# Kernel optimization log

Measured on AMD Instinct MI355X. Metric: run time of the kernel, lower is better.

The kernel has to match this reference:

```python
import jax, jax.numpy as jnp
import numpy as np

N_USERS = 100000
N_ITEMS = 50000
N_NODES = N_USERS + N_ITEMS
D = 32
N_EDGES = 8000000
N_LAYERS = 3
B = 65536


def setup_inputs() -> dict:
    key = jax.random.key(0)
    ks = jax.random.split(key, 9)
    users = jax.random.randint(ks[0], (B,), 0, N_USERS)
    items = jax.random.randint(ks[1], (B,), 0, N_ITEMS)
    # COO sparse normalized adjacency (symmetric bipartite graph in LightGCN)
    rows = jax.random.randint(ks[2], (N_EDGES,), 0, N_NODES)
    cols = jax.random.randint(ks[3], (N_EDGES,), 0, N_NODES)
    # normalized values ~ 1/sqrt(deg_i*deg_j); keep small so propagation is stable
    vals = jax.random.uniform(ks[4], (N_EDGES,), dtype=jnp.float32) * 0.01
    # embedding tables, init std=0.1 per nn.init.normal_(std=0.1)
    user_emb = jax.random.normal(ks[5], (N_USERS, D), dtype=jnp.float32) * 0.1
    item_emb = jax.random.normal(ks[6], (N_ITEMS, D), dtype=jnp.float32) * 0.1
    # per-user denormalization stats (norm_mode='users')
    norm_means = jax.random.normal(ks[7], (N_USERS,), dtype=jnp.float32)
    norm_stds = jax.random.uniform(ks[8], (N_USERS,), dtype=jnp.float32) + 0.5
    return {
        "users": users, "items": items,
        "rows": rows, "cols": cols, "vals": vals,
        "user_emb": user_emb, "item_emb": item_emb,
        "norm_means": norm_means, "norm_stds": norm_stds,
    }


def _spmm(rows, cols, vals, x):
    # sparse COO matmul: out[i] = sum_{e: rows[e]==i} vals[e] * x[cols[e]]
    return jax.ops.segment_sum(vals[:, None] * x[cols], rows, num_segments=N_NODES)


def reference(users, items, rows, cols, vals, user_emb, item_emb, norm_means, norm_stds):
    all_emb = jnp.concatenate([user_emb, item_emb], axis=0)  # [N, D]
    acc = all_emb
    emb_sum = all_emb
    for _ in range(N_LAYERS):
        acc = _spmm(rows, cols, vals, acc)
        emb_sum = emb_sum + acc
    light_out = emb_sum / jnp.asarray(N_LAYERS + 1, dtype=all_emb.dtype)
    all_users = light_out[:N_USERS]
    all_items = light_out[N_USERS:]
    gamma = jnp.sum(all_users[users] * all_items[items], axis=1)  # [B]
    # norm_mode == 'users' -> index stats by users
    return gamma * norm_stds[users] + norm_means[users]
```

## Files before the change

### kernel.cpp

```cpp
#include <hip/hip_runtime.h>
#include <hip/hip_fp16.h>

#define N_USERS 100000
#define N_ITEMS 50000
#define N_NODES 150000
#define DIM 32
#define N_EDGES 8000000
#define B_OUT 65536

#define NB 1024
#define RPB 147
#define CH 8192
#define N_PBLK ((N_EDGES + CH - 1) / CH)
#define PART_T 1024
#define EPT (CH / PART_T)
#define MS_T 1024
#define T 256
#define NRED 8
#define NPANEL 3
#define NBIN (RPB * NPANEL)
#define BUFE 8448
#define VQ_SCALE 1638400.0f
#define VQ_INV   6.103515625e-7f
#define WSCALE1 (VQ_INV * 8.0f)
#define WSCALE2 (VQ_INV * 32.0f)
#define WSCALE3 (VQ_INV * 32.0f)
#define INV1 (1.0f / 64.0f)
#define INV2 (1.0f / 2048.0f)
#define INV3 (1.0f / 65536.0f)

__device__ __forceinline__ unsigned enc_h(unsigned u16) {
    return (u16 + 0x7Fu + ((u16 >> 8) & 1u)) >> 8;
}
__device__ __forceinline__ unsigned enc_f(float x) {
    return enc_h((unsigned)__half_as_ushort(__float2half(x)));
}
__device__ __forceinline__ float dec_b(unsigned b) {
    return __half2float(__ushort_as_half((unsigned short)(b << 8)));
}
__device__ __forceinline__ int panel_of(int col) {
    return (col >= 100000) ? 2 : ((col >= 50000) ? 1 : 0);
}
__device__ __forceinline__ int chend(int c) {
    int e = (c + 1) * CH;
    return (e > N_EDGES) ? N_EDGES : e;
}

__global__ void init_kernel(const float* __restrict__ user_emb,
                            const float* __restrict__ item_emb,
                            unsigned char* __restrict__ x_a) {
    int i = blockIdx.x * blockDim.x + threadIdx.x;
    const int total = N_NODES * DIM / 8;
    if (i >= total) return;
    const int user8 = N_USERS * DIM / 8;
    const float4* src = (i < user8) ? ((const float4*)user_emb + (size_t)i * 2)
                                    : ((const float4*)item_emb + (size_t)(i - user8) * 2);
    float4 a = src[0], b = src[1];
    unsigned w0 = enc_f(a.x * 8.f) | (enc_f(a.y * 8.f) << 8)
                | (enc_f(a.z * 8.f) << 16) | (enc_f(a.w * 8.f) << 24);
    unsigned w1 = enc_f(b.x * 8.f) | (enc_f(b.y * 8.f) << 8)
                | (enc_f(b.z * 8.f) << 16) | (enc_f(b.w * 8.f) << 24);
    uint2 o; o.x = w0; o.y = w1;
    ((uint2*)x_a)[i] = o;
}

__global__ void __launch_bounds__(PART_T)
part_kernel(const int* __restrict__ rows,
            const int* __restrict__ cols,
            const float* __restrict__ vals,
            int* __restrict__ rsA,
            int2* __restrict__ bucket_ev) {
    __shared__ int2 buf[CH];
    __shared__ int hist[NB];
    __shared__ int wsum[16];
    const int tid   = threadIdx.x;
    const int chunk = blockIdx.x;
    const int e0    = chunk * CH;
    const int ecnt  = (N_EDGES - e0 < CH) ? (N_EDGES - e0) : CH;
    const int lane  = tid & 63, wid = tid >> 6;

    hist[tid] = 0;
    __syncthreads();

    int myrow[EPT];
    #pragma unroll
    for (int j = 0; j < EPT; ++j) {
        int idx = j * PART_T + tid;
        int r = (idx < ecnt) ? rows[e0 + idx] : -1;
        myrow[j] = r;
        if (r >= 0) atomicAdd(&hist[(unsigned)r / RPB], 1);
    }
    __syncthreads();

    int v = hist[tid];
    int inc = v;
    #pragma unroll
    for (int off = 1; off < 64; off <<= 1) {
        int t = __shfl_up(inc, off, 64);
        if (lane >= off) inc += t;
    }
    if (lane == 63) wsum[wid] = inc;
    __syncthreads();
    if (wid == 0) {
        int s = (lane < 16) ? wsum[lane] : 0;
        #pragma unroll
        for (int off = 1; off < 16; off <<= 1) {
            int t = __shfl_up(s, off, 64);
            if (lane >= off) s += t;
        }
        if (lane < 16) wsum[lane] = s;
    }
    __syncthreads();
    int base = (wid > 0) ? wsum[wid - 1] : 0;
    int excl = base + inc - v;
    rsA[(size_t)chunk * NB + tid] = e0 + excl;
    hist[tid] = excl;
    __syncthreads();

    #pragma unroll
    for (int j = 0; j < EPT; ++j) {
        int r = myrow[j];
        if (r < 0) continue;
        int idx = j * PART_T + tid;
        unsigned b = (unsigned)r / RPB;
        int k = atomicAdd(&hist[b], 1);
        int2 ev;
        ev.x = (int)(((unsigned)(r - (int)b * RPB) << 18) | (unsigned)cols[e0 + idx]);
        ev.y = __float_as_int(vals[e0 + idx]);
        buf[k] = ev;
    }
    __syncthreads();

    const int n4 = ecnt >> 1;
    const int4* b4 = (const int4*)buf;
    int4* g4 = (int4*)(bucket_ev + e0);
    for (int i = tid; i < n4; i += PART_T) g4[i] = b4[i];
}

__global__ void transpose_kernel(const int* __restrict__ in, int* __restrict__ out) {
    __shared__ int t[32][33];
    const int c0 = blockIdx.x * 32, b0 = blockIdx.y * 32;
    for (int dy = threadIdx.y; dy < 32; dy += 8) {
        int c = c0 + dy, b = b0 + threadIdx.x;
        t[dy][threadIdx.x] = (c < N_PBLK) ? in[(size_t)c * NB + b] : 0;
    }
    __syncthreads();
    for (int dy = threadIdx.y; dy < 32; dy += 8) {
        int b = b0 + dy, c = c0 + threadIdx.x;
        if (c < N_PBLK) out[(size_t)b * N_PBLK + c] = t[threadIdx.x][dy];
    }
}

__global__ void btot_kernel(const int* __restrict__ rsA, int* __restrict__ partial) {
    const int b = threadIdx.x;
    const int g = blockIdx.x;
    int c = 0;
    for (int ch = g; ch < N_PBLK; ch += NRED) {
        int s0 = rsA[(size_t)ch * NB + b];
        int s1 = (b < NB - 1) ? rsA[(size_t)ch * NB + b + 1] : chend(ch);
        c += s1 - s0;
    }
    partial[g * NB + b] = c;
}

__global__ void bscan_kernel(const int* __restrict__ partial,
                             int* __restrict__ bcsr,
                             int* __restrict__ row_ptr) {
    __shared__ int wsum[16];
    const int tid = threadIdx.x;
    const int lane = tid & 63, wid = tid >> 6;
    int v = 0;
    #pragma unroll
    for (int g = 0; g < NRED; ++g) v += partial[g * NB + tid];
    int inc = v;
    #pragma unroll
    for (int off = 1; off < 64; off <<= 1) {
        int t = __shfl_up(inc, off, 64);
        if (lane >= off) inc += t;
    }
    if (lane == 63) wsum[wid] = inc;
    __syncthreads();
    if (wid == 0) {
        int s = (lane < 16) ? wsum[lane] : 0;
        #pragma unroll
        for (int off = 1; off < 16; off <<= 1) {
            int t = __shfl_up(s, off, 64);
            if (lane >= off) s += t;
        }
        if (lane < 16) wsum[lane] = s;
    }
    __syncthreads();
    int base = (wid > 0) ? wsum[wid - 1] : 0;
    bcsr[tid] = base + inc - v;
    if (tid == 0) row_ptr[N_NODES] = N_EDGES;
}

__global__ void __launch_bounds__(MS_T)
mini_scatter_kernel(const int* __restrict__ rsT,
                    const int2* __restrict__ bucket_ev,
                    const int* __restrict__ bcsr,
                    int* __restrict__ row_ptr,
                    unsigned* __restrict__ csr_w) {
    __shared__ int2 ibuf[BUFE];
    __shared__ unsigned sbuf[BUFE];
    __shared__ int rs0[N_PBLK];
    __shared__ int ofs[N_PBLK];
    __shared__ int rlen[N_PBLK];
    __shared__ int cnt2[NBIN];
    __shared__ int cur2[NBIN];
    __shared__ int wsum[MS_T / 64];
    const int b   = blockIdx.x;
    const int tid = threadIdx.x;
    const int lane = tid & 63, wid = tid >> 6;

    for (int i = tid; i < N_PBLK; i += MS_T) {
        int a = rsT[(size_t)b * N_PBLK + i];
        int e = (b < NB - 1) ? rsT[(size_t)(b + 1) * N_PBLK + i]
                             : chend(i);
        rs0[i]  = a;
        rlen[i] = e - a;
    }
    if (tid < NBIN) cnt2[tid] = 0;
    __syncthreads();

    int lv = (tid < N_PBLK) ? rlen[tid] : 0;
    int linc = lv;
    #pragma unroll
    for (int off = 1; off < 64; off <<= 1) {
        int t = __shfl_up(linc, off, 64);
        if (lane >= off) linc += t;
    }
    if (lane == 63) wsum[wid] = linc;
    __syncthreads();
    if (wid == 0) {
        int s = (lane < MS_T / 64) ? wsum[lane] : 0;
        #pragma unroll
        for (int off = 1; off < MS_T / 64; off <<= 1) {
            int t = __shfl_up(s, off, 64);
            if (lane >= off) s += t;
        }
        if (lane < MS_T / 64) wsum[lane] = s;
    }
    __syncthreads();
    int lbase = (wid > 0) ? wsum[wid - 1] : 0;
    if (tid < N_PBLK) ofs[tid] = lbase + linc - lv;
    __syncthreads();
    const int cnt = ofs[N_PBLK - 1] + rlen[N_PBLK - 1];
    __syncthreads();

    const int grp8 = tid >> 3, ln8 = tid & 7;
    const int cb = bcsr[b];

    if (cnt <= BUFE) {
        for (int c = grp8; c < N_PBLK; c += (MS_T / 8)) {
            int s0 = rs0[c], o0 = ofs[c], L = rlen[c];
            for (int i = ln8; i < L; i += 8) ibuf[o0 + i] = bucket_ev[s0 + i];
        }
        __syncthreads();
        for (int i = tid; i < cnt; i += MS_T) {
            unsigned key = (unsigned)ibuf[i].x;
            atomicAdd(&cnt2[((int)(key >> 18)) * NPANEL + panel_of((int)(key & 0x3FFFFu))], 1);
        }
    } else {
        for (int c = grp8; c < N_PBLK; c += (MS_T / 8)) {
            int s0 = rs0[c], L = rlen[c];
            for (int i = ln8; i < L; i += 8) {
                unsigned key = (unsigned)bucket_ev[s0 + i].x;
                atomicAdd(&cnt2[((int)(key >> 18)) * NPANEL + panel_of((int)(key & 0x3FFFFu))], 1);
            }
        }
    }
    __syncthreads();

    int v = (tid < NBIN) ? cnt2[tid] : 0;
    int inc = v;
    #pragma unroll
    for (int off = 1; off < 64; off <<= 1) {
        int t = __shfl_up(inc, off, 64);
        if (lane >= off) inc += t;
    }
    if (lane == 63) wsum[wid] = inc;
    __syncthreads();
    if (wid == 0) {
        int s = (lane < MS_T / 64) ? wsum[lane] : 0;
        #pragma unroll
        for (int off = 1; off < MS_T / 64; off <<= 1) {
            int t = __shfl_up(s, off, 64);
            if (lane >= off) s += t;
        }
        if (lane < MS_T / 64) wsum[lane] = s;
    }
    __syncthreads();
    int base = (wid > 0) ? wsum[wid - 1] : 0;
    if (tid < NBIN) {
        int excl = base + inc - v;
        cur2[tid] = excl;
        if (tid % NPANEL == 0) {
            int r = b * RPB + tid / NPANEL;
            if (r < N_NODES) row_ptr[r] = cb + excl;
        }
    }
    __syncthreads();

    if (cnt <= BUFE) {
        for (int i = tid; i < cnt; i += MS_T) {
            int2 ev = ibuf[i];
            unsigned key = (unsigned)ev.x;
            int rl  = (int)(key >> 18);
            int col = (int)(key & 0x3FFFFu);
            float vv = __int_as_float(ev.y);
            int q = (int)(vv * VQ_SCALE + 0.5f);
            if (q > 16383) q = 16383;
            int pos = atomicAdd(&cur2[rl * NPANEL + panel_of(col)], 1);
            sbuf[pos] = ((unsigned)col << 14) | (unsigned)q;
        }
        __syncthreads();
        unsigned* g = csr_w + cb;
        for (int i = tid; i < cnt; i += MS_T) g[i] = sbuf[i];
    } else {
        for (int c = grp8; c < N_PBLK; c += (MS_T / 8)) {
            int s0 = rs0[c], L = rlen[c];
            for (int i = ln8; i < L; i += 8) {
                int2 ev = bucket_ev[s0 + i];
                unsigned key = (unsigned)ev.x;
                int rl  = (int)(key >> 18);
                int col = (int)(key & 0x3FFFFu);
                float vv = __int_as_float(ev.y);
                int q = (int)(vv * VQ_SCALE + 0.5f);
                if (q > 16383) q = 16383;
                int pos = atomicAdd(&cur2[rl * NPANEL + panel_of(col)], 1);
                csr_w[cb + pos] = ((unsigned)col << 14) | (unsigned)q;
            }
        }
    }
}

__global__ void spmm_kernel(const int* __restrict__ row_ptr,
                            const unsigned* __restrict__ csr,
                            const unsigned char* __restrict__ xin,
                            unsigned char* __restrict__ xout,
                            float wscale) {
    int tid = blockIdx.x * blockDim.x + threadIdx.x;
    int row = tid >> 5;
    if (row >= N_NODES) return;
    const int ll  = tid & 31;
    const int j   = ll >> 2;
    const int seg = ll & 3;
    const int s = row_ptr[row];
    const int e = row_ptr[row + 1];
    const unsigned char* xseg = xin + seg * 8;

    __half2 acc0 = __float2half2_rn(0.f);
    __half2 acc1 = acc0, acc2 = acc0, acc3 = acc0;

    for (int i = s; i < e; i += 32) {
        int e0 = i + j, e1 = i + 8 + j, e2 = i + 16 + j, e3 = i + 24 + j;
        unsigned p0 = (e0 < e) ? csr[e0] : 0u;
        unsigned p1 = (e1 < e) ? csr[e1] : 0u;
        unsigned p2 = (e2 < e) ? csr[e2] : 0u;
        unsigned p3 = (e3 < e) ? csr[e3] : 0u;
        uint2 v0 = *(const uint2*)(xseg + ((size_t)((p0 >> 9) & ~31u)));
        uint2 v1 = *(const uint2*)(xseg + ((size_t)((p1 >> 9) & ~31u)));
        uint2 v2 = *(const uint2*)(xseg + ((size_t)((p2 >> 9) & ~31u)));
        uint2 v3 = *(const uint2*)(xseg + ((size_t)((p3 >> 9) & ~31u)));
        __half2 w0 = __float2half2_rn((float)(p0 & 0x3FFFu) * wscale);
        __half2 w1 = __float2half2_rn((float)(p1 & 0x3FFFu) * wscale);
        __half2 w2 = __float2half2_rn((float)(p2 & 0x3FFFu) * wscale);
        __half2 w3 = __float2half2_rn((float)(p3 & 0x3FFFu) * wscale);
        unsigned h;
        h = __builtin_amdgcn_perm(v0.x, v0.x, 0x010C000Cu);
        acc0 = __hfma2(w0, *(__half2*)&h, acc0);
        h = __builtin_amdgcn_perm(v0.x, v0.x, 0x030C020Cu);
        acc1 = __hfma2(w0, *(__half2*)&h, acc1);
        h = __builtin_amdgcn_perm(v0.y, v0.y, 0x010C000Cu);
        acc2 = __hfma2(w0, *(__half2*)&h, acc2);
        h = __builtin_amdgcn_perm(v0.y, v0.y, 0x030C020Cu);
        acc3 = __hfma2(w0, *(__half2*)&h, acc3);
        h = __builtin_amdgcn_perm(v1.x, v1.x, 0x010C000Cu);
        acc0 = __hfma2(w1, *(__half2*)&h, acc0);
        h = __builtin_amdgcn_perm(v1.x, v1.x, 0x030C020Cu);
        acc1 = __hfma2(w1, *(__half2*)&h, acc1);
        h = __builtin_amdgcn_perm(v1.y, v1.y, 0x010C000Cu);
        acc2 = __hfma2(w1, *(__half2*)&h, acc2);
        h = __builtin_amdgcn_perm(v1.y, v1.y, 0x030C020Cu);
        acc3 = __hfma2(w1, *(__half2*)&h, acc3);
        h = __builtin_amdgcn_perm(v2.x, v2.x, 0x010C000Cu);
        acc0 = __hfma2(w2, *(__half2*)&h, acc0);
        h = __builtin_amdgcn_perm(v2.x, v2.x, 0x030C020Cu);
        acc1 = __hfma2(w2, *(__half2*)&h, acc1);
        h = __builtin_amdgcn_perm(v2.y, v2.y, 0x010C000Cu);
        acc2 = __hfma2(w2, *(__half2*)&h, acc2);
        h = __builtin_amdgcn_perm(v2.y, v2.y, 0x030C020Cu);
        acc3 = __hfma2(w2, *(__half2*)&h, acc3);
        h = __builtin_amdgcn_perm(v3.x, v3.x, 0x010C000Cu);
        acc0 = __hfma2(w3, *(__half2*)&h, acc0);
        h = __builtin_amdgcn_perm(v3.x, v3.x, 0x030C020Cu);
        acc1 = __hfma2(w3, *(__half2*)&h, acc1);
        h = __builtin_amdgcn_perm(v3.y, v3.y, 0x010C000Cu);
        acc2 = __hfma2(w3, *(__half2*)&h, acc2);
        h = __builtin_amdgcn_perm(v3.y, v3.y, 0x030C020Cu);
        acc3 = __hfma2(w3, *(__half2*)&h, acc3);
    }

    #pragma unroll
    for (int m = 4; m <= 16; m <<= 1) {
        unsigned t;
        t = (unsigned)__shfl_xor(*(int*)&acc0, m, 64); acc0 = __hadd2(acc0, *(__half2*)&t);
        t = (unsigned)__shfl_xor(*(int*)&acc1, m, 64); acc1 = __hadd2(acc1, *(__half2*)&t);
        t = (unsigned)__shfl_xor(*(int*)&acc2, m, 64); acc2 = __hadd2(acc2, *(__half2*)&t);
        t = (unsigned)__shfl_xor(*(int*)&acc3, m, 64); acc3 = __hadd2(acc3, *(__half2*)&t);
    }

    if (j == 0) {
        unsigned a0 = *(unsigned*)&acc0, a1 = *(unsigned*)&acc1;
        unsigned a2 = *(unsigned*)&acc2, a3 = *(unsigned*)&acc3;
        unsigned w0 = enc_h(a0 & 0xFFFFu) | (enc_h(a0 >> 16) << 8)
                    | (enc_h(a1 & 0xFFFFu) << 16) | (enc_h(a1 >> 16) << 24);
        unsigned w1 = enc_h(a2 & 0xFFFFu) | (enc_h(a2 >> 16) << 8)
                    | (enc_h(a3 & 0xFFFFu) << 16) | (enc_h(a3 >> 16) << 24);
        uint2 o; o.x = w0; o.y = w1;
        *(uint2*)(xout + (size_t)row * 32 + seg * 8) = o;
    }
}

__device__ __forceinline__ void add_row8(float* s, const unsigned char* x,
                                         size_t node, float inv) {
    const uint4* p = (const uint4*)(x + node * 32);
    uint4 t0 = p[0], t1 = p[1];
    unsigned w[8] = {t0.x, t0.y, t0.z, t0.w, t1.x, t1.y, t1.z, t1.w};
    #pragma unroll
    for (int k = 0; k < 8; ++k) {
        unsigned ww = w[k];
        s[k * 4 + 0] += dec_b(ww & 0xFFu) * inv;
        s[k * 4 + 1] += dec_b((ww >> 8) & 0xFFu) * inv;
        s[k * 4 + 2] += dec_b((ww >> 16) & 0xFFu) * inv;
        s[k * 4 + 3] += dec_b(ww >> 24) * inv;
    }
}

__global__ void final_kernel(const int* __restrict__ users,
                             const int* __restrict__ items,
                             const float* __restrict__ user_emb,
                             const float* __restrict__ item_emb,
                             const unsigned char* __restrict__ x1,
                             const unsigned char* __restrict__ x2,
                             const unsigned char* __restrict__ x3,
                             const float* __restrict__ means,
                             const float* __restrict__ stds,
                             float* __restrict__ out) {
    int b = blockIdx.x * blockDim.x + threadIdx.x;
    if (b >= B_OUT) return;
    int u  = users[b];
    int itm = items[b];
    size_t un = (size_t)u;
    size_t in = (size_t)(N_USERS + itm);

    float su[DIM], si[DIM];
    const float4* eu = (const float4*)(user_emb + un * DIM);
    const float4* ei = (const float4*)(item_emb + (size_t)itm * DIM);
    #pragma unroll
    for (int k = 0; k < 8; ++k) {
        float4 a = eu[k];
        su[k * 4 + 0] = a.x; su[k * 4 + 1] = a.y; su[k * 4 + 2] = a.z; su[k * 4 + 3] = a.w;
        float4 c = ei[k];
        si[k * 4 + 0] = c.x; si[k * 4 + 1] = c.y; si[k * 4 + 2] = c.z; si[k * 4 + 3] = c.w;
    }
    add_row8(su, x1, un, INV1); add_row8(su, x2, un, INV2); add_row8(su, x3, un, INV3);
    add_row8(si, x1, in, INV1); add_row8(si, x2, in, INV2); add_row8(si, x3, in, INV3);

    float gamma = 0.f;
    #pragma unroll
    for (int d = 0; d < DIM; ++d) gamma += su[d] * si[d];
    gamma *= 0.0625f;
    out[b] = gamma * stds[u] + means[u];
}

extern "C" void kernel_launch(void* const* d_in, const int* in_sizes, int n_in,
                              void* d_out, int out_size, void* d_ws, size_t ws_size,
                              hipStream_t stream) {
    const int*   users    = (const int*)d_in[0];
    const int*   items    = (const int*)d_in[1];
    const int*   rows     = (const int*)d_in[2];
    const int*   cols     = (const int*)d_in[3];
    const float* vals     = (const float*)d_in[4];
    const float* user_emb = (const float*)d_in[5];
    const float* item_emb = (const float*)d_in[6];
    const float* means    = (const float*)d_in[7];
    const float* stds     = (const float*)d_in[8];
    float* out = (float*)d_out;

    char* w = (char*)d_ws;
    size_t off = 0;
    auto alloc = [&](size_t bytes) -> void* {
        void* p = w + off;
        off = (off + bytes + 255) & ~(size_t)255;
        return p;
    };
    size_t regionA = ((size_t)N_PBLK * CH * sizeof(int2) + 255) & ~(size_t)255;
    char* a0 = (char*)alloc(regionA);
    int2* bucket_ev = (int2*)a0;
    size_t aoff = 0;
    auto allocA = [&](size_t bytes) -> void* {
        void* p = a0 + aoff;
        aoff = (aoff + bytes + 255) & ~(size_t)255;
        return p;
    };
    unsigned char* x_a = (unsigned char*)allocA((size_t)N_NODES * DIM);
    unsigned char* x_b = (unsigned char*)allocA((size_t)N_NODES * DIM);
    unsigned char* x_c = (unsigned char*)allocA((size_t)N_NODES * DIM);
    unsigned char* x_d = (unsigned char*)allocA((size_t)N_NODES * DIM);

    int*      rsA     = (int*)     alloc((size_t)N_PBLK * NB * sizeof(int));
    int*      rsT     = (int*)     alloc((size_t)NB * N_PBLK * sizeof(int));
    int*      partial = (int*)     alloc((size_t)NRED * NB * sizeof(int));
    int*      row_ptr = (int*)     alloc((size_t)(N_NODES + 1) * sizeof(int));
    int*      bcsr    = (int*)     alloc((size_t)NB * sizeof(int));
    unsigned* csr_w   = (unsigned*)alloc((size_t)N_EDGES * sizeof(unsigned));
    (void)ws_size;

    const int g_init  = (N_NODES * DIM / 8 + T - 1) / T;
    const int g_spmm  = (N_NODES * DIM + T - 1) / T;
    const int g_final = (B_OUT + T - 1) / T;

    part_kernel<<<N_PBLK, PART_T, 0, stream>>>(rows, cols, vals, rsA, bucket_ev);
    dim3 tgrid((N_PBLK + 31) / 32, NB / 32);
    transpose_kernel<<<tgrid, dim3(32, 8), 0, stream>>>(rsA, rsT);
    btot_kernel<<<NRED, NB, 0, stream>>>(rsA, partial);
    bscan_kernel<<<1, NB, 0, stream>>>(partial, bcsr, row_ptr);
    mini_scatter_kernel<<<NB, MS_T, 0, stream>>>(rsT, bucket_ev, bcsr, row_ptr, csr_w);

    init_kernel<<<g_init, T, 0, stream>>>(user_emb, item_emb, x_a);
    spmm_kernel<<<g_spmm, T, 0, stream>>>(row_ptr, csr_w, x_a, x_b, WSCALE1);
    spmm_kernel<<<g_spmm, T, 0, stream>>>(row_ptr, csr_w, x_b, x_c, WSCALE2);
    spmm_kernel<<<g_spmm, T, 0, stream>>>(row_ptr, csr_w, x_c, x_d, WSCALE3);

    final_kernel<<<g_final, T, 0, stream>>>(users, items, user_emb, item_emb,
                                            x_b, x_c, x_d, means, stds, out);
}
```

Measured before the change: 297.1 us.

## Split 8-bit embeddings into two 16-dim planes and run SpMM per plane

Stores each layer's quantized 32-dim embeddings as two separate planes of 16 bytes per node and launches the SpMM twice per layer, once per plane. Each pass gathers a smaller working set (2.4 MB per plane), so the randomly gathered rows should fit better in cache and each 32-lane group covers twice as many edges per iteration. The cost is reading the CSR indices and weights twice per layer, plus twice as many launches. The init and final kernels are updated to the new plane layout.

New measurement: 378.3 us. 27.3% more time.

```diff
diff --git a/kernel.cpp b/kernel.cpp
--- a/kernel.cpp
+++ b/kernel.cpp
@@ -28,6 +28,7 @@
 #define INV1 (1.0f / 64.0f)
 #define INV2 (1.0f / 2048.0f)
 #define INV3 (1.0f / 65536.0f)
+#define PLANE ((size_t)N_NODES * 16)
 
 __device__ __forceinline__ unsigned enc_h(unsigned u16) {
     return (u16 + 0x7Fu + ((u16 >> 8) & 1u)) >> 8;
@@ -60,8 +61,10 @@
                 | (enc_f(a.z * 8.f) << 16) | (enc_f(a.w * 8.f) << 24);
     unsigned w1 = enc_f(b.x * 8.f) | (enc_f(b.y * 8.f) << 8)
                 | (enc_f(b.z * 8.f) << 16) | (enc_f(b.w * 8.f) << 24);
+    int node = i >> 2, k = i & 3;
+    unsigned char* dst = x_a + (size_t)(k >> 1) * PLANE + (size_t)node * 16 + (k & 1) * 8;
     uint2 o; o.x = w0; o.y = w1;
-    ((uint2*)x_a)[i] = o;
+    *(uint2*)dst = o;
 }
 
 __global__ void __launch_bounds__(PART_T)
@@ -215,8 +218,7 @@
 
     for (int i = tid; i < N_PBLK; i += MS_T) {
         int a = rsT[(size_t)b * N_PBLK + i];
-        int e = (b < NB - 1) ? rsT[(size_t)(b + 1) * N_PBLK + i]
-                             : chend(i);
+        int e = (b < NB - 1) ? rsT[(size_t)(b + 1) * N_PBLK + i] : chend(i);
         rs0[i]  = a;
         rlen[i] = e - a;
     }
@@ -344,8 +346,8 @@
     int row = tid >> 5;
     if (row >= N_NODES) return;
     const int ll  = tid & 31;
-    const int j   = ll >> 2;
-    const int seg = ll & 3;
+    const int j   = ll >> 1;
+    const int seg = ll & 1;
     const int s = row_ptr[row];
     const int e = row_ptr[row + 1];
     const unsigned char* xseg = xin + seg * 8;
@@ -353,16 +355,16 @@
     __half2 acc0 = __float2half2_rn(0.f);
     __half2 acc1 = acc0, acc2 = acc0, acc3 = acc0;
 
-    for (int i = s; i < e; i += 32) {
-        int e0 = i + j, e1 = i + 8 + j, e2 = i + 16 + j, e3 = i + 24 + j;
+    for (int i = s; i < e; i += 64) {
+        int e0 = i + j, e1 = i + 16 + j, e2 = i + 32 + j, e3 = i + 48 + j;
         unsigned p0 = (e0 < e) ? csr[e0] : 0u;
         unsigned p1 = (e1 < e) ? csr[e1] : 0u;
         unsigned p2 = (e2 < e) ? csr[e2] : 0u;
         unsigned p3 = (e3 < e) ? csr[e3] : 0u;
-        uint2 v0 = *(const uint2*)(xseg + ((size_t)((p0 >> 9) & ~31u)));
-        uint2 v1 = *(const uint2*)(xseg + ((size_t)((p1 >> 9) & ~31u)));
-        uint2 v2 = *(const uint2*)(xseg + ((size_t)((p2 >> 9) & ~31u)));
-        uint2 v3 = *(const uint2*)(xseg + ((size_t)((p3 >> 9) & ~31u)));
+        uint2 v0 = *(const uint2*)(xseg + ((size_t)((p0 >> 10) & ~15u)));
+        uint2 v1 = *(const uint2*)(xseg + ((size_t)((p1 >> 10) & ~15u)));
+        uint2 v2 = *(const uint2*)(xseg + ((size_t)((p2 >> 10) & ~15u)));
+        uint2 v3 = *(const uint2*)(xseg + ((size_t)((p3 >> 10) & ~15u)));
         __half2 w0 = __float2half2_rn((float)(p0 & 0x3FFFu) * wscale);
         __half2 w1 = __float2half2_rn((float)(p1 & 0x3FFFu) * wscale);
         __half2 w2 = __float2half2_rn((float)(p2 & 0x3FFFu) * wscale);
@@ -403,7 +405,7 @@
     }
 
     #pragma unroll
-    for (int m = 4; m <= 16; m <<= 1) {
+    for (int m = 2; m <= 16; m <<= 1) {
         unsigned t;
         t = (unsigned)__shfl_xor(*(int*)&acc0, m, 64); acc0 = __hadd2(acc0, *(__half2*)&t);
         t = (unsigned)__shfl_xor(*(int*)&acc1, m, 64); acc1 = __hadd2(acc1, *(__half2*)&t);
@@ -419,17 +421,16 @@
         unsigned w1 = enc_h(a2 & 0xFFFFu) | (enc_h(a2 >> 16) << 8)
                     | (enc_h(a3 & 0xFFFFu) << 16) | (enc_h(a3 >> 16) << 24);
         uint2 o; o.x = w0; o.y = w1;
-        *(uint2*)(xout + (size_t)row * 32 + seg * 8) = o;
-    }
-}
-
-__device__ __forceinline__ void add_row8(float* s, const unsigned char* x,
-                                         size_t node, float inv) {
-    const uint4* p = (const uint4*)(x + node * 32);
-    uint4 t0 = p[0], t1 = p[1];
-    unsigned w[8] = {t0.x, t0.y, t0.z, t0.w, t1.x, t1.y, t1.z, t1.w};
-    #pragma unroll
-    for (int k = 0; k < 8; ++k) {
+        *(uint2*)(xout + (size_t)row * 16 + seg * 8) = o;
+    }
+}
+
+__device__ __forceinline__ void add_plane(float* s, const unsigned char* xp,
+                                          size_t node, float inv) {
+    uint4 t = *(const uint4*)(xp + node * 16);
+    unsigned w[4] = {t.x, t.y, t.z, t.w};
+    #pragma unroll
+    for (int k = 0; k < 4; ++k) {
         unsigned ww = w[k];
         s[k * 4 + 0] += dec_b(ww & 0xFFu) * inv;
         s[k * 4 + 1] += dec_b((ww >> 8) & 0xFFu) * inv;
@@ -465,8 +466,12 @@
         float4 c = ei[k];
         si[k * 4 + 0] = c.x; si[k * 4 + 1] = c.y; si[k * 4 + 2] = c.z; si[k * 4 + 3] = c.w;
     }
-    add_row8(su, x1, un, INV1); add_row8(su, x2, un, INV2); add_row8(su, x3, un, INV3);
-    add_row8(si, x1, in, INV1); add_row8(si, x2, in, INV2); add_row8(si, x3, in, INV3);
+    add_plane(su,      x1,         un, INV1); add_plane(su + 16, x1 + PLANE, un, INV1);
+    add_plane(su,      x2,         un, INV2); add_plane(su + 16, x2 + PLANE, un, INV2);
+    add_plane(su,      x3,         un, INV3); add_plane(su + 16, x3 + PLANE, un, INV3);
+    add_plane(si,      x1,         in, INV1); add_plane(si + 16, x1 + PLANE, in, INV1);
+    add_plane(si,      x2,         in, INV2); add_plane(si + 16, x2 + PLANE, in, INV2);
+    add_plane(si,      x3,         in, INV3); add_plane(si + 16, x3 + PLANE, in, INV3);
 
     float gamma = 0.f;
     #pragma unroll
@@ -505,10 +510,10 @@
         aoff = (aoff + bytes + 255) & ~(size_t)255;
         return p;
     };
-    unsigned char* x_a = (unsigned char*)allocA((size_t)N_NODES * DIM);
-    unsigned char* x_b = (unsigned char*)allocA((size_t)N_NODES * DIM);
-    unsigned char* x_c = (unsigned char*)allocA((size_t)N_NODES * DIM);
-    unsigned char* x_d = (unsigned char*)allocA((size_t)N_NODES * DIM);
+    unsigned char* x_a = (unsigned char*)allocA(2 * PLANE);
+    unsigned char* x_b = (unsigned char*)allocA(2 * PLANE);
+    unsigned char* x_c = (unsigned char*)allocA(2 * PLANE);
+    unsigned char* x_d = (unsigned char*)allocA(2 * PLANE);
 
     int*      rsA     = (int*)     alloc((size_t)N_PBLK * NB * sizeof(int));
     int*      rsT     = (int*)     alloc((size_t)NB * N_PBLK * sizeof(int));
@@ -530,9 +535,15 @@
     mini_scatter_kernel<<<NB, MS_T, 0, stream>>>(rsT, bucket_ev, bcsr, row_ptr, csr_w);
 
     init_kernel<<<g_init, T, 0, stream>>>(user_emb, item_emb, x_a);
-    spmm_kernel<<<g_spmm, T, 0, stream>>>(row_ptr, csr_w, x_a, x_b, WSCALE1);
-    spmm_kernel<<<g_spmm, T, 0, stream>>>(row_ptr, csr_w, x_b, x_c, WSCALE2);
-    spmm_kernel<<<g_spmm, T, 0, stream>>>(row_ptr, csr_w, x_c, x_d, WSCALE3);
+
+    unsigned char* lay[4] = {x_a, x_b, x_c, x_d};
+    float ws[3] = {WSCALE1, WSCALE2, WSCALE3};
+    for (int l = 0; l < 3; ++l) {
+        unsigned char* xi = lay[l];
+        unsigned char* xo = lay[l + 1];
+        spmm_kernel<<<g_spmm, T, 0, stream>>>(row_ptr, csr_w, xi,         xo,         ws[l]);
+        spmm_kernel<<<g_spmm, T, 0, stream>>>(row_ptr, csr_w, xi + PLANE, xo + PLANE, ws[l]);
+    }
 
     final_kernel<<<g_final, T, 0, stream>>>(users, items, user_emb, item_emb,
                                             x_b, x_c, x_d, means, stds, out);
```
